# Optimization experiments

Hardware: AMD Instinct MI355X
Metric: run time of the kernel (lower is better)

Reference implementation:

```python
import jax, jax.numpy as jnp
import numpy as np

D = 512; L = 8; NH = 8; BS = 32; HW = 32; VA = 8; HA = 8; SEQ = 2 * VA * HA
DK = D // NH  # per-head dim
LN_EPS = 1e-5


def setup_inputs() -> dict:
    key = jax.random.key(0)
    ks = iter(jax.random.split(key, 40))
    def rn(shape, s=0.02):
        return (s * jax.random.normal(next(ks), shape)).astype(jnp.float32)
    inp = {
        'rgb_fea': jax.random.normal(next(ks), (BS, D, HW, HW), jnp.float32),
        'ir_fea':  jax.random.normal(next(ks), (BS, D, HW, HW), jnp.float32),
        'pos_emb': rn((1, SEQ, D)),
        'conv1_w': rn((8, D), 0.05),    # 1x1 conv, stored [out,in]
        'conv2_w': rn((D, 8), 0.05),
        'ln1_w': jnp.ones((L, D)), 'ln1_b': jnp.zeros((L, D)),
        'Wq': rn((L, D, D)), 'bq': jnp.zeros((L, D)),
        'Wk': rn((L, D, D)), 'bk': jnp.zeros((L, D)),
        'Wv': rn((L, D, D)), 'bv': jnp.zeros((L, D)),
        'Wo': rn((L, D, D)), 'bo': jnp.zeros((L, D)),
        'ln2_w': jnp.ones((L, D)), 'ln2_b': jnp.zeros((L, D)),
        'W1': rn((L, D, 4 * D)), 'b1': jnp.zeros((L, 4 * D)),
        'W2': rn((L, 4 * D, D)), 'b2': jnp.zeros((L, D)),
        'lnf_w': jnp.ones((D,)), 'lnf_b': jnp.zeros((D,)),
    }
    return inp


def _ln(x, w, b):
    m = x.mean(-1, keepdims=True)
    v = jnp.var(x, axis=-1, keepdims=True)
    return (x - m) / jnp.sqrt(v + LN_EPS) * w + b


def _avgpool8(x):
    b, c, h, w = x.shape
    return x.reshape(b, c, VA, h // VA, HA, w // HA).mean(axis=(3, 5))


def _highpass(x):
    # extract_frequency2: fftshifted FFT, zero the [crow-thr:crow+thr, ccol-thr:ccol+thr]
    # block (Python slice semantics, negative start wraps), then inverse FFT.
    rows, cols = x.shape[-2], x.shape[-1]
    crow, ccol = rows // 2, cols // 2
    thr = crow + ccol // 4
    f = jnp.fft.fftshift(jnp.fft.fftn(x, axes=(-2, -1)), axes=(-2, -1))
    f = f.at[:, :, crow - thr:crow + thr, ccol - thr:ccol + thr].set(0)
    hp = jnp.fft.ifftn(jnp.fft.ifftshift(f, axes=(-2, -1)), axes=(-2, -1))
    return hp.real  # real part (torch code casts to half; real part is the runnable interpretation)


def _block(x, p):
    ln1 = _ln(x, p['ln1_w'], p['ln1_b'])
    q = (ln1 @ p['Wq'] + p['bq']).reshape(BS, SEQ, NH, DK).transpose(0, 2, 1, 3)
    k = (ln1 @ p['Wk'] + p['bk']).reshape(BS, SEQ, NH, DK).transpose(0, 2, 1, 3)
    v = (ln1 @ p['Wv'] + p['bv']).reshape(BS, SEQ, NH, DK).transpose(0, 2, 1, 3)
    att = jax.nn.softmax(jnp.einsum('bhqd,bhkd->bhqk', q, k) / np.sqrt(DK), axis=-1)
    o = jnp.einsum('bhqk,bhkd->bhqd', att, v).transpose(0, 2, 1, 3).reshape(BS, SEQ, D)
    x = x + o @ p['Wo'] + p['bo']
    ln2 = _ln(x, p['ln2_w'], p['ln2_b'])
    h = jax.nn.gelu(ln2 @ p['W1'] + p['b1'], approximate=False)
    x = x + h @ p['W2'] + p['b2']
    return x, None


def reference(rgb_fea, ir_fea, pos_emb, conv1_w, conv2_w, ln1_w, ln1_b,
              Wq, bq, Wk, bk, Wv, bv, Wo, bo, ln2_w, ln2_b,
              W1, b1, W2, b2, lnf_w, lnf_b):
    bs, c, h, w = rgb_fea.shape
    rgb_p = _avgpool8(rgb_fea)
    ir_p = _avgpool8(ir_fea)
    rgb_hp = _highpass(rgb_p)
    ir_hp = _highpass(ir_p)

    conv1 = lambda t: jnp.einsum('bchw,oc->bohw', t, conv1_w)
    rgb_hp_M = jax.nn.sigmoid(conv1(rgb_hp * rgb_p))
    ir_hp_M = jax.nn.sigmoid(conv1(ir_hp * ir_p))
    rgb_M = jax.nn.sigmoid(conv1(rgb_p))
    ir_M = jax.nn.sigmoid(conv1(ir_p))

    hw = VA * HA
    half = (bs * 8) // 8  # = bs
    M = jnp.concatenate([rgb_M.reshape(-1, hw), ir_M.reshape(-1, hw),
                         rgb_hp_M.reshape(-1, hw)[:half], ir_hp_M.reshape(-1, hw)[:half]], axis=0)
    l = M.shape[0]
    s = M.sum(0)
    # sum_{i<j} M_i . M_j = (||sum_i M_i||^2 - sum_i ||M_i||^2) / 2
    patten_loss = (jnp.dot(s, s) - jnp.sum(M * M)) * 0.5 / (l * (l - 1))

    P_rgb = jnp.einsum('bchw,oc->bohw', rgb_M, conv2_w) * rgb_p
    P_ir = jnp.einsum('bchw,oc->bohw', ir_M, conv2_w) * ir_p

    tok = jnp.concatenate([P_rgb.reshape(bs, c, -1), P_ir.reshape(bs, c, -1)], axis=2)
    x = pos_emb + tok.transpose(0, 2, 1)  # [bs, 2*VA*HA, d]

    layer = {'ln1_w': ln1_w, 'ln1_b': ln1_b, 'Wq': Wq, 'bq': bq, 'Wk': Wk, 'bk': bk,
             'Wv': Wv, 'bv': bv, 'Wo': Wo, 'bo': bo, 'ln2_w': ln2_w, 'ln2_b': ln2_b,
             'W1': W1, 'b1': b1, 'W2': W2, 'b2': b2}
    x, _ = jax.lax.scan(_block, x, layer)
    x = _ln(x, lnf_w, lnf_b)

    x = x.reshape(bs, 2, VA, HA, D).transpose(0, 1, 4, 2, 3)  # [bs,2,d,VA,HA]
    rgb_out = jax.image.resize(x[:, 0], (bs, D, h, w), method='bilinear')
    ir_out = jax.image.resize(x[:, 1], (bs, D, h, w), method='bilinear')
    return rgb_out, ir_out, patten_loss
```

## Files before the change

kernel.cpp:

```cpp
#include <hip/hip_runtime.h>
#include <math.h>

typedef unsigned short u16;
typedef short v8s __attribute__((ext_vector_type(8)));
typedef float v4f __attribute__((ext_vector_type(4)));

#define MTOT 4096

__device__ __forceinline__ u16 f2bf(float f) {
  unsigned int u = __float_as_uint(f);
  u += 0x7fffu + ((u >> 16) & 1u);
  return (u16)(u >> 16);
}

__device__ __forceinline__ v4f mfma16(v8s a, v8s b, v4f c) {
  return __builtin_amdgcn_mfma_f32_16x16x32_bf16(a, b, c, 0, 0, 0);
}

__device__ __forceinline__ void gl_lds16(const u16* g, u16* l) {
  __builtin_amdgcn_global_load_lds(
      (const __attribute__((address_space(1))) void*)g,
      (__attribute__((address_space(3))) void*)l, 16, 0, 0);
}

__constant__ float c_ct[8] = {1.f, -0.70710678118654752f, 0.f, 0.70710678118654752f,
                              -1.f, 0.70710678118654752f, 0.f, -0.70710678118654752f};
__constant__ float c_st[8] = {0.f, 0.70710678118654752f, -1.f, 0.70710678118654752f,
                              0.f, -0.70710678118654752f, 1.f, -0.70710678118654752f};

__global__ __launch_bounds__(256) void transpose_bf16_kernel(
    const float* __restrict__ src, u16* __restrict__ dst,
    int K, int N, size_t srcLS, size_t dstLS, int rowOff)
{
  int l = blockIdx.z;
  int n0 = blockIdx.x * 32, k0 = blockIdx.y * 32;
  __shared__ float tile[32][33];
  int tx = threadIdx.x & 31, ty = threadIdx.x >> 5;
  const float* s = src + (size_t)l * srcLS;
#pragma unroll
  for (int rr = 0; rr < 4; ++rr) {
    int k = k0 + ty + rr * 8;
    tile[ty + rr * 8][tx] = s[(size_t)k * N + n0 + tx];
  }
  __syncthreads();
  u16* dp = dst + (size_t)l * dstLS;
#pragma unroll
  for (int rr = 0; rr < 4; ++rr) {
    int n = n0 + ty + rr * 8;
    dp[(size_t)(rowOff + n) * K + k0 + tx] = f2bf(tile[tx][ty + rr * 8]);
  }
}

__global__ __launch_bounds__(256) void qkv_transpose_kernel(
    const float* __restrict__ Wq, const float* __restrict__ Wk,
    const float* __restrict__ Wv, u16* __restrict__ dst)
{
  int z = blockIdx.z;
  int l = z / 3, which = z % 3;
  const float* src = (which == 0) ? Wq : (which == 1) ? Wk : Wv;
  int n0 = blockIdx.x * 32, k0 = blockIdx.y * 32;
  __shared__ float tile[32][33];
  int tx = threadIdx.x & 31, ty = threadIdx.x >> 5;
  const float* s = src + (size_t)l * 512 * 512;
#pragma unroll
  for (int rr = 0; rr < 4; ++rr) {
    int k = k0 + ty + rr * 8;
    tile[ty + rr * 8][tx] = s[(size_t)k * 512 + n0 + tx];
  }
  __syncthreads();
  u16* dp = dst + (size_t)l * 1536 * 512;
  int rowOff = which * 512;
#pragma unroll
  for (int rr = 0; rr < 4; ++rr) {
    int n = n0 + ty + rr * 8;
    dp[(size_t)(rowOff + n) * 512 + k0 + tx] = f2bf(tile[tx][ty + rr * 8]);
  }
}

__global__ __launch_bounds__(256) void qkvbias_kernel(
    const float* __restrict__ bq, const float* __restrict__ bk,
    const float* __restrict__ bv, float* __restrict__ qb)
{
  int l = blockIdx.x;
  for (int j = threadIdx.x; j < 1536; j += 256) {
    float v = (j < 512) ? bq[l * 512 + j] : (j < 1024) ? bk[l * 512 + j - 512] : bv[l * 512 + j - 1024];
    qb[l * 1536 + j] = v;
  }
}

__global__ __launch_bounds__(256) void pool_kernel(
    const float* __restrict__ rgb, const float* __restrict__ ir, float* __restrict__ pool)
{
  int idx = blockIdx.x * 4 + (threadIdx.x >> 6);
  int i = threadIdx.x & 63;
  int y = i >> 3, xcol = i & 7;
  int timg = idx >> 14;
  int rem = idx & 16383;
  const float* src = (timg ? ir : rgb) + (size_t)rem * 1024;
  float s = 0.f;
#pragma unroll
  for (int r = 0; r < 4; ++r) {
    float4 v = *(const float4*)(src + (y * 4 + r) * 32 + xcol * 4);
    s += v.x + v.y + v.z + v.w;
  }
  pool[(size_t)idx * 64 + i] = s * 0.0625f;
}

__global__ __launch_bounds__(256) void convm_kernel(
    const float* __restrict__ pool, const float* __restrict__ conv1_w,
    float* __restrict__ Macc)
{
  int r = blockIdx.x;
  int cc = blockIdx.y;
  int t = threadIdx.x, hw = t & 63, cg = t >> 6;
  int kind = (r < 64) ? 0 : 1;
  int prow;
  if (kind == 0) prow = r;
  else { int rh = r - 64; prow = (rh >> 2) * 32 + (rh & 3); }
  int yy = hw >> 3, xx = hw & 7;
  int sd = (yy + xx) & 7;
  float ct = c_ct[sd], st = c_st[sd];
  float acc[8] = {0.f,0.f,0.f,0.f,0.f,0.f,0.f,0.f};
  const float* pbase = pool + ((size_t)prow * 512 + cc * 64) * 64;
#pragma unroll 4
  for (int it = 0; it < 16; ++it) {
    int cl = cg * 16 + it;
    int c = cc * 64 + cl;
    float p = pbase[(size_t)cl * 64 + hw];
    float val = p;
    if (kind == 1) {
      float C = p * ct, S = p * st;
#pragma unroll
      for (int d = 1; d < 64; d <<= 1) { C += __shfl_xor(C, d, 64); S += __shfl_xor(S, d, 64); }
      float hp = p - (C * ct + S * st) * (1.0f / 64.0f);
      val = hp * p;
    }
#pragma unroll
    for (int o = 0; o < 8; ++o) acc[o] += conv1_w[o * 512 + c] * val;
  }
  __shared__ float red[4][8][64];
#pragma unroll
  for (int o = 0; o < 8; ++o) red[cg][o][hw] = acc[o];
  __syncthreads();
  if (cg == 0) {
#pragma unroll
    for (int o = 0; o < 8; ++o) {
      float s = red[0][o][hw] + red[1][o][hw] + red[2][o][hw] + red[3][o][hw];
      Macc[((size_t)cc * 72 + r) * 512 + o * 64 + hw] = s;
    }
  }
}

__global__ __launch_bounds__(256) void msig_kernel(
    const float* __restrict__ Macc, float* __restrict__ Mplain, float* __restrict__ Mhp)
{
  int i = blockIdx.x * 256 + threadIdx.x;
  float s = 0.f;
#pragma unroll
  for (int cc = 0; cc < 8; ++cc) s += Macc[(size_t)cc * 72 * 512 + i];
  float m = 1.0f / (1.0f + expf(-s));
  if (i < 64 * 512) Mplain[i] = m;
  else Mhp[i - 64 * 512] = m;
}

__global__ __launch_bounds__(256) void loss_kernel(
    const float* __restrict__ Mplain, const float* __restrict__ Mhp, float* __restrict__ out)
{
  int t = threadIdx.x, col = t & 63, rg = t >> 6;
  float sp = 0.f, sq = 0.f;
  for (int r = rg; r < 576; r += 4) {
    const float* rowp = (r < 512) ? (Mplain + (size_t)r * 64) : (Mhp + (size_t)(r - 512) * 64);
    float v = rowp[col];
    sp += v; sq += v * v;
  }
  __shared__ float scol[4][64], ssq[4][64];
  scol[rg][col] = sp; ssq[rg][col] = sq;
  __syncthreads();
  if (t < 64) {
    float s = scol[0][t] + scol[1][t] + scol[2][t] + scol[3][t];
    float q = ssq[0][t] + ssq[1][t] + ssq[2][t] + ssq[3][t];
    float ds = s * s;
#pragma unroll
    for (int d = 1; d < 64; d <<= 1) { ds += __shfl_xor(ds, d, 64); q += __shfl_xor(q, d, 64); }
    if (t == 0) *out = (ds - q) * 0.5f / (576.0f * 575.0f);
  }
}

__global__ __launch_bounds__(256) void token_kernel(
    const float* __restrict__ pos_emb, const float* __restrict__ conv2_w,
    const float* __restrict__ Mplain, const float* __restrict__ pool, float* __restrict__ x)
{
  int bs_idx = blockIdx.x;
  int b = bs_idx >> 7, s = bs_idx & 127;
  int timg = s >> 6, hw = s & 63;
  __shared__ float Ms[8];
  if (threadIdx.x < 8)
    Ms[threadIdx.x] = Mplain[((size_t)(timg * 32 + b) * 8 + threadIdx.x) * 64 + hw];
  __syncthreads();
#pragma unroll
  for (int i = 0; i < 2; ++i) {
    int d = threadIdx.x + i * 256;
    float acc = 0.f;
#pragma unroll
    for (int o = 0; o < 8; ++o) acc += conv2_w[d * 8 + o] * Ms[o];
    float p = pool[(((size_t)timg * 32 + b) * 512 + d) * 64 + hw];
    x[(size_t)bs_idx * 512 + d] = pos_emb[s * 512 + d] + acc * p;
  }
}

template<int OBF>
__global__ __launch_bounds__(256) void ln_kernel(
    const float* __restrict__ xin, const float* __restrict__ w,
    const float* __restrict__ bb, void* __restrict__ out)
{
  int row = blockIdx.x, t = threadIdx.x;
  float2 v = ((const float2*)(xin + (size_t)row * 512))[t];
  float s = v.x + v.y, q = v.x * v.x + v.y * v.y;
#pragma unroll
  for (int d = 1; d < 64; d <<= 1) { s += __shfl_xor(s, d, 64); q += __shfl_xor(q, d, 64); }
  __shared__ float ps[4], pq[4];
  int wv = t >> 6;
  if ((t & 63) == 0) { ps[wv] = s; pq[wv] = q; }
  __syncthreads();
  float S = ps[0] + ps[1] + ps[2] + ps[3];
  float Q = pq[0] + pq[1] + pq[2] + pq[3];
  float mean = S * (1.0f / 512.0f);
  float var = Q * (1.0f / 512.0f) - mean * mean;
  float rstd = rsqrtf(var + 1e-5f);
  float o0 = (v.x - mean) * rstd * w[t * 2] + bb[t * 2];
  float o1 = (v.y - mean) * rstd * w[t * 2 + 1] + bb[t * 2 + 1];
  if (OBF) { u16* o = (u16*)out + (size_t)row * 512; o[t * 2] = f2bf(o0); o[t * 2 + 1] = f2bf(o1); }
  else     { float* o = (float*)out + (size_t)row * 512; o[t * 2] = o0; o[t * 2 + 1] = o1; }
}

template<int ACT, int RESID, int OBF>
__global__ __launch_bounds__(256) void gemm_bt(
    const u16* __restrict__ A, const u16* __restrict__ BT,
    const float* __restrict__ bias, const float* __restrict__ resid,
    void* __restrict__ Cout, int N, int K)
{
  __shared__ u16 As[128 * 32];
  __shared__ u16 Bs[128 * 32];
  const int m0 = blockIdx.y * 128, n0 = blockIdx.x * 128;
  const int t = threadIdx.x, lane = t & 63, w = t >> 6;
  const int lr = lane & 15, lq = lane >> 4;
  const int wm = (w & 1) * 64, wn = (w >> 1) * 64;
  v4f acc[4][4];
  const v4f vzero = {0.f, 0.f, 0.f, 0.f};
#pragma unroll
  for (int mt = 0; mt < 4; ++mt)
#pragma unroll
    for (int nt = 0; nt < 4; ++nt) acc[mt][nt] = vzero;

  for (int kk = 0; kk < K; kk += 32) {
    __syncthreads();
    {
      int r0 = t >> 2, c0 = (t & 3) << 3;
      gl_lds16(A  + (size_t)(m0 + r0) * K + kk + c0, As + (size_t)(w * 64) * 8);
      gl_lds16(BT + (size_t)(n0 + r0) * K + kk + c0, Bs + (size_t)(w * 64) * 8);
      int ch = 256 + t;
      int r1 = ch >> 2, c1 = (ch & 3) << 3;
      gl_lds16(A  + (size_t)(m0 + r1) * K + kk + c1, As + (size_t)(256 + w * 64) * 8);
      gl_lds16(BT + (size_t)(n0 + r1) * K + kk + c1, Bs + (size_t)(256 + w * 64) * 8);
    }
    __syncthreads();
    v8s a[4], b[4];
#pragma unroll
    for (int mt = 0; mt < 4; ++mt)
      a[mt] = *(const v8s*)(As + (wm + mt * 16 + lr) * 32 + lq * 8);
#pragma unroll
    for (int nt = 0; nt < 4; ++nt)
      b[nt] = *(const v8s*)(Bs + (wn + nt * 16 + lr) * 32 + lq * 8);
#pragma unroll
    for (int mt = 0; mt < 4; ++mt)
#pragma unroll
      for (int nt = 0; nt < 4; ++nt)
        acc[mt][nt] = mfma16(a[mt], b[nt], acc[mt][nt]);
  }

#pragma unroll
  for (int mt = 0; mt < 4; ++mt)
#pragma unroll
    for (int nt = 0; nt < 4; ++nt) {
      int col = n0 + wn + nt * 16 + lr;
      float bsv = bias[col];
#pragma unroll
      for (int r = 0; r < 4; ++r) {
        int row = m0 + wm + mt * 16 + lq * 4 + r;
        float v = acc[mt][nt][r] + bsv;
        if (ACT == 1) v = 0.5f * v * (1.0f + erff(v * 0.70710678118654752f));
        if (RESID) v += resid[(size_t)row * N + col];
        if (OBF) ((u16*)Cout)[(size_t)row * N + col] = f2bf(v);
        else     ((float*)Cout)[(size_t)row * N + col] = v;
      }
    }
}

template<int ACT, int RESID, int OBF>
__global__ __launch_bounds__(256) void gemm_bt64(
    const u16* __restrict__ A, const u16* __restrict__ BT,
    const float* __restrict__ bias, const float* __restrict__ resid,
    void* __restrict__ Cout, int N, int K)
{
  __shared__ u16 As[128 * 32];
  __shared__ u16 Bs[64 * 32];
  const int m0 = blockIdx.y * 128, n0 = blockIdx.x * 64;
  const int t = threadIdx.x, lane = t & 63, w = t >> 6;
  const int lr = lane & 15, lq = lane >> 4;
  const int wm = (w & 1) * 64, wn = (w >> 1) * 32;
  v4f acc[4][2];
  const v4f vzero = {0.f, 0.f, 0.f, 0.f};
#pragma unroll
  for (int mt = 0; mt < 4; ++mt)
#pragma unroll
    for (int nt = 0; nt < 2; ++nt) acc[mt][nt] = vzero;

  for (int kk = 0; kk < K; kk += 32) {
    __syncthreads();
    {
      int r0 = t >> 2, c0 = (t & 3) << 3;
      gl_lds16(A  + (size_t)(m0 + r0) * K + kk + c0, As + (size_t)(w * 64) * 8);
      gl_lds16(BT + (size_t)(n0 + r0) * K + kk + c0, Bs + (size_t)(w * 64) * 8);
      int ch = 256 + t;
      int r1 = ch >> 2, c1 = (ch & 3) << 3;
      gl_lds16(A  + (size_t)(m0 + r1) * K + kk + c1, As + (size_t)(256 + w * 64) * 8);
    }
    __syncthreads();
    v8s a[4], b[2];
#pragma unroll
    for (int mt = 0; mt < 4; ++mt)
      a[mt] = *(const v8s*)(As + (wm + mt * 16 + lr) * 32 + lq * 8);
#pragma unroll
    for (int nt = 0; nt < 2; ++nt)
      b[nt] = *(const v8s*)(Bs + (wn + nt * 16 + lr) * 32 + lq * 8);
#pragma unroll
    for (int mt = 0; mt < 4; ++mt)
#pragma unroll
      for (int nt = 0; nt < 2; ++nt)
        acc[mt][nt] = mfma16(a[mt], b[nt], acc[mt][nt]);
  }

#pragma unroll
  for (int mt = 0; mt < 4; ++mt)
#pragma unroll
    for (int nt = 0; nt < 2; ++nt) {
      int col = n0 + wn + nt * 16 + lr;
      float bsv = bias[col];
#pragma unroll
      for (int r = 0; r < 4; ++r) {
        int row = m0 + wm + mt * 16 + lq * 4 + r;
        float v = acc[mt][nt][r] + bsv;
        if (ACT == 1) v = 0.5f * v * (1.0f + erff(v * 0.70710678118654752f));
        if (RESID) v += resid[(size_t)row * N + col];
        if (OBF) ((u16*)Cout)[(size_t)row * N + col] = f2bf(v);
        else     ((float*)Cout)[(size_t)row * N + col] = v;
      }
    }
}

__global__ __launch_bounds__(256) void attn_kernel(
    const u16* __restrict__ qkv, u16* __restrict__ attn_out)
{
  __shared__ u16 Ks[128 * 64];
  __shared__ u16 Vt[64 * 128];
  __shared__ u16 Ps[128 * 128];
  const int h = blockIdx.x, b = blockIdx.y;
  const int t = threadIdx.x, lane = t & 63, w = t >> 6;
  const int lr = lane & 15, lq = lane >> 4;
  const u16* base = qkv + (size_t)b * 128 * 1536 + h * 64;

#pragma unroll
  for (int i = 0; i < 4; ++i) {
    int ch = i * 256 + t;
    int s = ch >> 3, off = (ch & 7) * 8;
    *(v8s*)(Ks + s * 64 + off) = *(const v8s*)(base + 512 + (size_t)s * 1536 + off);
    v8s vv = *(const v8s*)(base + 1024 + (size_t)s * 1536 + off);
#pragma unroll
    for (int j = 0; j < 8; ++j) Vt[(off + j) * 128 + s] = (u16)vv[j];
  }
  __syncthreads();

  const v4f vzero = {0.f, 0.f, 0.f, 0.f};
  v4f sacc[2][8];
#pragma unroll
  for (int mt = 0; mt < 2; ++mt)
#pragma unroll
    for (int nt = 0; nt < 8; ++nt) sacc[mt][nt] = vzero;
#pragma unroll
  for (int kk = 0; kk < 64; kk += 32) {
    v8s a0 = *(const v8s*)(base + (size_t)(w * 32 + lr) * 1536 + kk + lq * 8);
    v8s a1 = *(const v8s*)(base + (size_t)(w * 32 + 16 + lr) * 1536 + kk + lq * 8);
#pragma unroll
    for (int nt = 0; nt < 8; ++nt) {
      v8s bb = *(const v8s*)(Ks + (nt * 16 + lr) * 64 + kk + lq * 8);
      sacc[0][nt] = mfma16(a0, bb, sacc[0][nt]);
      sacc[1][nt] = mfma16(a1, bb, sacc[1][nt]);
    }
  }

  float rinv[2][4];
#pragma unroll
  for (int mt = 0; mt < 2; ++mt)
#pragma unroll
    for (int r = 0; r < 4; ++r) {
      float mx = -3.0e38f;
#pragma unroll
      for (int nt = 0; nt < 8; ++nt) mx = fmaxf(mx, sacc[mt][nt][r]);
#pragma unroll
      for (int d = 1; d < 16; d <<= 1) mx = fmaxf(mx, __shfl_xor(mx, d, 64));
      float ls = 0.f;
      float pv[8];
#pragma unroll
      for (int nt = 0; nt < 8; ++nt) {
        pv[nt] = expf((sacc[mt][nt][r] - mx) * 0.125f);
        ls += pv[nt];
      }
#pragma unroll
      for (int d = 1; d < 16; d <<= 1) ls += __shfl_xor(ls, d, 64);
      rinv[mt][r] = 1.0f / ls;
      int row = w * 32 + mt * 16 + lq * 4 + r;
#pragma unroll
      for (int nt = 0; nt < 8; ++nt) Ps[row * 128 + nt * 16 + lr] = f2bf(pv[nt]);
    }
  __syncthreads();

  v4f oacc[2][4];
#pragma unroll
  for (int mt = 0; mt < 2; ++mt)
#pragma unroll
    for (int nt = 0; nt < 4; ++nt) oacc[mt][nt] = vzero;
#pragma unroll
  for (int kk = 0; kk < 128; kk += 32) {
    v8s a0 = *(const v8s*)(Ps + (w * 32 + lr) * 128 + kk + lq * 8);
    v8s a1 = *(const v8s*)(Ps + (w * 32 + 16 + lr) * 128 + kk + lq * 8);
#pragma unroll
    for (int nt = 0; nt < 4; ++nt) {
      v8s bb = *(const v8s*)(Vt + (nt * 16 + lr) * 128 + kk + lq * 8);
      oacc[0][nt] = mfma16(a0, bb, oacc[0][nt]);
      oacc[1][nt] = mfma16(a1, bb, oacc[1][nt]);
    }
  }
#pragma unroll
  for (int mt = 0; mt < 2; ++mt)
#pragma unroll
    for (int nt = 0; nt < 4; ++nt)
#pragma unroll
      for (int r = 0; r < 4; ++r) {
        int row = w * 32 + mt * 16 + lq * 4 + r;
        int col = nt * 16 + lr;
        attn_out[((size_t)(b * 128 + row)) * 512 + h * 64 + col] =
            f2bf(oacc[mt][nt][r] * rinv[mt][r]);
      }
}

__global__ __launch_bounds__(256) void upsample_kernel(
    const float* __restrict__ xf, float* __restrict__ out)
{
  int bid = blockIdx.x;
  int c = bid & 511;
  int tb = bid >> 9;
  int b = tb & 31, timg = tb >> 5;
  __shared__ float tile[64];
  if (threadIdx.x < 64) {
    int s = timg * 64 + threadIdx.x;
    tile[threadIdx.x] = xf[((size_t)b * 128 + s) * 512 + c];
  }
  __syncthreads();
  float* obase = out + (size_t)timg * (32ull * 512 * 1024) + ((size_t)b * 512 + c) * 1024;
#pragma unroll
  for (int k = 0; k < 4; ++k) {
    int pix = threadIdx.x + k * 256;
    int i = pix >> 5, j = pix & 31;
    float cy = fminf(fmaxf((i - 1.5f) * 0.25f, 0.f), 7.f);
    float cx = fminf(fmaxf((j - 1.5f) * 0.25f, 0.f), 7.f);
    int y0 = (int)cy, x0 = (int)cx;
    int y1 = min(y0 + 1, 7), x1 = min(x0 + 1, 7);
    float fy = cy - y0, fx = cx - x0;
    float v00 = tile[y0 * 8 + x0], v01 = tile[y0 * 8 + x1];
    float v10 = tile[y1 * 8 + x0], v11 = tile[y1 * 8 + x1];
    obase[pix] = (v00 * (1.f - fx) + v01 * fx) * (1.f - fy) + (v10 * (1.f - fx) + v11 * fx) * fy;
  }
}

extern "C" void kernel_launch(void* const* d_in, const int* in_sizes, int n_in,
                              void* d_out, int out_size, void* d_ws, size_t ws_size,
                              hipStream_t stream)
{
  const float* rgb_fea = (const float*)d_in[0];
  const float* ir_fea  = (const float*)d_in[1];
  const float* pos_emb = (const float*)d_in[2];
  const float* conv1_w = (const float*)d_in[3];
  const float* conv2_w = (const float*)d_in[4];
  const float* ln1_w = (const float*)d_in[5];
  const float* ln1_b = (const float*)d_in[6];
  const float* Wq = (const float*)d_in[7];
  const float* bq = (const float*)d_in[8];
  const float* Wk = (const float*)d_in[9];
  const float* bk = (const float*)d_in[10];
  const float* Wv = (const float*)d_in[11];
  const float* bv = (const float*)d_in[12];
  const float* Wo = (const float*)d_in[13];
  const float* bo = (const float*)d_in[14];
  const float* ln2_w = (const float*)d_in[15];
  const float* ln2_b = (const float*)d_in[16];
  const float* W1 = (const float*)d_in[17];
  const float* b1 = (const float*)d_in[18];
  const float* W2 = (const float*)d_in[19];
  const float* b2 = (const float*)d_in[20];
  const float* lnf_w = (const float*)d_in[21];
  const float* lnf_b = (const float*)d_in[22];
  (void)in_sizes; (void)n_in; (void)out_size; (void)ws_size;

  char* wsb = (char*)d_ws;
  size_t off = 0;
  auto alloc = [&](size_t nbytes) -> void* {
    void* p = wsb + off;
    off += (nbytes + 255) & ~(size_t)255;
    return p;
  };
  float* pool   = (float*)alloc(2ull * 32 * 512 * 64 * 4);
  float* Macc   = (float*)alloc(8ull * 72 * 512 * 4);
  float* Mplain = (float*)alloc(2ull * 32 * 8 * 64 * 4);
  float* Mhp    = (float*)alloc(2ull * 4 * 8 * 64 * 4);
  float* x      = (float*)alloc((size_t)MTOT * 512 * 4);
  float* xf     = (float*)alloc((size_t)MTOT * 512 * 4);
  u16* ln_out   = (u16*)alloc((size_t)MTOT * 512 * 2);
  u16* qkv      = (u16*)alloc((size_t)MTOT * 1536 * 2);
  u16* attn     = (u16*)alloc((size_t)MTOT * 512 * 2);
  u16* hbuf     = (u16*)alloc((size_t)MTOT * 2048 * 2);
  u16* WqkvT    = (u16*)alloc(8ull * 1536 * 512 * 2);
  u16* WoT      = (u16*)alloc(8ull * 512 * 512 * 2);
  u16* W1T      = (u16*)alloc(8ull * 2048 * 512 * 2);
  u16* W2T      = (u16*)alloc(8ull * 512 * 2048 * 2);
  float* qb     = (float*)alloc(8ull * 1536 * 4);

  qkv_transpose_kernel<<<dim3(16, 16, 24), 256, 0, stream>>>(Wq, Wk, Wv, WqkvT);
  transpose_bf16_kernel<<<dim3(16, 16, 8), 256, 0, stream>>>(Wo, WoT, 512, 512, 512ull * 512, 512ull * 512, 0);
  transpose_bf16_kernel<<<dim3(64, 16, 8), 256, 0, stream>>>(W1, W1T, 512, 2048, 512ull * 2048, 2048ull * 512, 0);
  transpose_bf16_kernel<<<dim3(16, 64, 8), 256, 0, stream>>>(W2, W2T, 2048, 512, 2048ull * 512, 512ull * 2048, 0);
  qkvbias_kernel<<<8, 256, 0, stream>>>(bq, bk, bv, qb);

  pool_kernel<<<8192, 256, 0, stream>>>(rgb_fea, ir_fea, pool);
  convm_kernel<<<dim3(72, 8), 256, 0, stream>>>(pool, conv1_w, Macc);
  msig_kernel<<<144, 256, 0, stream>>>(Macc, Mplain, Mhp);
  loss_kernel<<<1, 256, 0, stream>>>(Mplain, Mhp, (float*)d_out + 33554432);
  token_kernel<<<MTOT, 256, 0, stream>>>(pos_emb, conv2_w, Mplain, pool, x);

  for (int l = 0; l < 8; ++l) {
    ln_kernel<1><<<MTOT, 256, 0, stream>>>(x, ln1_w + l * 512, ln1_b + l * 512, ln_out);
    gemm_bt<0, 0, 1><<<dim3(12, 32), 256, 0, stream>>>(
        ln_out, WqkvT + (size_t)l * 1536 * 512, qb + l * 1536, nullptr, qkv, 1536, 512);
    attn_kernel<<<dim3(8, 32), 256, 0, stream>>>(qkv, attn);
    gemm_bt64<0, 1, 0><<<dim3(8, 32), 256, 0, stream>>>(
        attn, WoT + (size_t)l * 512 * 512, bo + l * 512, x, x, 512, 512);
    ln_kernel<1><<<MTOT, 256, 0, stream>>>(x, ln2_w + l * 512, ln2_b + l * 512, ln_out);
    gemm_bt<1, 0, 1><<<dim3(16, 32), 256, 0, stream>>>(
        ln_out, W1T + (size_t)l * 2048 * 512, b1 + l * 2048, nullptr, hbuf, 2048, 512);
    gemm_bt64<0, 1, 0><<<dim3(8, 32), 256, 0, stream>>>(
        hbuf, W2T + (size_t)l * 512 * 2048, b2 + l * 512, x, x, 512, 2048);
  }

  ln_kernel<0><<<MTOT, 256, 0, stream>>>(x, lnf_w, lnf_b, xf);
  upsample_kernel<<<32768, 256, 0, stream>>>(xf, (float*)d_out);
}
```

Measured before the change: 1.374 ms.

## Widen GEMM K-step with XOR-swizzled LDS, tanh GELU, one-wave-per-row LayerNorm

```diff
diff --git a/kernel.cpp b/kernel.cpp
--- a/kernel.cpp
+++ b/kernel.cpp
@@ -3,6 +3,7 @@
 
 typedef unsigned short u16;
 typedef short v8s __attribute__((ext_vector_type(8)));
+typedef unsigned short v8u __attribute__((ext_vector_type(8)));
 typedef float v4f __attribute__((ext_vector_type(4)));
 
 #define MTOT 4096
@@ -21,6 +22,12 @@
   __builtin_amdgcn_global_load_lds(
       (const __attribute__((address_space(1))) void*)g,
       (__attribute__((address_space(3))) void*)l, 16, 0, 0);
+}
+
+__device__ __forceinline__ float fast_gelu(float v) {
+  float y = 0.7978845608028654f * (v + 0.044715f * v * v * v);
+  float t = 1.0f - 2.0f / (__expf(2.0f * y) + 1.0f);
+  return 0.5f * v * (1.0f + t);
 }
 
 __constant__ float c_ct[8] = {1.f, -0.70710678118654752f, 0.f, 0.70710678118654752f,
@@ -213,24 +220,38 @@
     const float* __restrict__ xin, const float* __restrict__ w,
     const float* __restrict__ bb, void* __restrict__ out)
 {
-  int row = blockIdx.x, t = threadIdx.x;
-  float2 v = ((const float2*)(xin + (size_t)row * 512))[t];
-  float s = v.x + v.y, q = v.x * v.x + v.y * v.y;
+  int wv = threadIdx.x >> 6, lane = threadIdx.x & 63;
+  int row = blockIdx.x * 4 + wv;
+  const float4* rp = (const float4*)(xin + (size_t)row * 512);
+  float4 v0 = rp[lane * 2], v1 = rp[lane * 2 + 1];
+  float s = v0.x + v0.y + v0.z + v0.w + v1.x + v1.y + v1.z + v1.w;
+  float q = v0.x*v0.x + v0.y*v0.y + v0.z*v0.z + v0.w*v0.w
+          + v1.x*v1.x + v1.y*v1.y + v1.z*v1.z + v1.w*v1.w;
 #pragma unroll
   for (int d = 1; d < 64; d <<= 1) { s += __shfl_xor(s, d, 64); q += __shfl_xor(q, d, 64); }
-  __shared__ float ps[4], pq[4];
-  int wv = t >> 6;
-  if ((t & 63) == 0) { ps[wv] = s; pq[wv] = q; }
-  __syncthreads();
-  float S = ps[0] + ps[1] + ps[2] + ps[3];
-  float Q = pq[0] + pq[1] + pq[2] + pq[3];
-  float mean = S * (1.0f / 512.0f);
-  float var = Q * (1.0f / 512.0f) - mean * mean;
+  float mean = s * (1.0f / 512.0f);
+  float var = q * (1.0f / 512.0f) - mean * mean;
   float rstd = rsqrtf(var + 1e-5f);
-  float o0 = (v.x - mean) * rstd * w[t * 2] + bb[t * 2];
-  float o1 = (v.y - mean) * rstd * w[t * 2 + 1] + bb[t * 2 + 1];
-  if (OBF) { u16* o = (u16*)out + (size_t)row * 512; o[t * 2] = f2bf(o0); o[t * 2 + 1] = f2bf(o1); }
-  else     { float* o = (float*)out + (size_t)row * 512; o[t * 2] = o0; o[t * 2 + 1] = o1; }
+  const float4* wp = (const float4*)w;
+  const float4* bp = (const float4*)bb;
+  float4 w0 = wp[lane * 2], w1 = wp[lane * 2 + 1];
+  float4 b0 = bp[lane * 2], b1 = bp[lane * 2 + 1];
+  float o0 = (v0.x - mean) * rstd * w0.x + b0.x;
+  float o1 = (v0.y - mean) * rstd * w0.y + b0.y;
+  float o2 = (v0.z - mean) * rstd * w0.z + b0.z;
+  float o3 = (v0.w - mean) * rstd * w0.w + b0.w;
+  float o4 = (v1.x - mean) * rstd * w1.x + b1.x;
+  float o5 = (v1.y - mean) * rstd * w1.y + b1.y;
+  float o6 = (v1.z - mean) * rstd * w1.z + b1.z;
+  float o7 = (v1.w - mean) * rstd * w1.w + b1.w;
+  if (OBF) {
+    v8u pk = { f2bf(o0), f2bf(o1), f2bf(o2), f2bf(o3), f2bf(o4), f2bf(o5), f2bf(o6), f2bf(o7) };
+    *(v8u*)((u16*)out + (size_t)row * 512 + lane * 8) = pk;
+  } else {
+    float4* op = (float4*)((float*)out + (size_t)row * 512);
+    op[lane * 2] = make_float4(o0, o1, o2, o3);
+    op[lane * 2 + 1] = make_float4(o4, o5, o6, o7);
+  }
 }
 
 template<int ACT, int RESID, int OBF>
@@ -239,8 +260,8 @@
     const float* __restrict__ bias, const float* __restrict__ resid,
     void* __restrict__ Cout, int N, int K)
 {
-  __shared__ u16 As[128 * 32];
-  __shared__ u16 Bs[128 * 32];
+  __shared__ u16 As[128 * 64];
+  __shared__ u16 Bs[128 * 64];
   const int m0 = blockIdx.y * 128, n0 = blockIdx.x * 128;
   const int t = threadIdx.x, lane = t & 63, w = t >> 6;
   const int lr = lane & 15, lq = lane >> 4;
@@ -252,30 +273,43 @@
 #pragma unroll
     for (int nt = 0; nt < 4; ++nt) acc[mt][nt] = vzero;
 
-  for (int kk = 0; kk < K; kk += 32) {
+  int srow[4], sgs[4];
+#pragma unroll
+  for (int i = 0; i < 4; ++i) {
+    int c = t + i * 256;
+    srow[i] = c >> 3;
+    sgs[i] = (c & 7) ^ (srow[i] & 7);
+  }
+
+  for (int kk = 0; kk < K; kk += 64) {
     __syncthreads();
-    {
-      int r0 = t >> 2, c0 = (t & 3) << 3;
-      gl_lds16(A  + (size_t)(m0 + r0) * K + kk + c0, As + (size_t)(w * 64) * 8);
-      gl_lds16(BT + (size_t)(n0 + r0) * K + kk + c0, Bs + (size_t)(w * 64) * 8);
-      int ch = 256 + t;
-      int r1 = ch >> 2, c1 = (ch & 3) << 3;
-      gl_lds16(A  + (size_t)(m0 + r1) * K + kk + c1, As + (size_t)(256 + w * 64) * 8);
-      gl_lds16(BT + (size_t)(n0 + r1) * K + kk + c1, Bs + (size_t)(256 + w * 64) * 8);
+#pragma unroll
+    for (int i = 0; i < 4; ++i) {
+      gl_lds16(A  + (size_t)(m0 + srow[i]) * K + kk + sgs[i] * 8, As + (size_t)(w * 64 + i * 256) * 8);
+      gl_lds16(BT + (size_t)(n0 + srow[i]) * K + kk + sgs[i] * 8, Bs + (size_t)(w * 64 + i * 256) * 8);
     }
     __syncthreads();
-    v8s a[4], b[4];
-#pragma unroll
-    for (int mt = 0; mt < 4; ++mt)
-      a[mt] = *(const v8s*)(As + (wm + mt * 16 + lr) * 32 + lq * 8);
-#pragma unroll
-    for (int nt = 0; nt < 4; ++nt)
-      b[nt] = *(const v8s*)(Bs + (wn + nt * 16 + lr) * 32 + lq * 8);
-#pragma unroll
-    for (int mt = 0; mt < 4; ++mt)
-#pragma unroll
-      for (int nt = 0; nt < 4; ++nt)
-        acc[mt][nt] = mfma16(a[mt], b[nt], acc[mt][nt]);
+#pragma unroll
+    for (int ks = 0; ks < 2; ++ks) {
+      v8s a[4], b[4];
+#pragma unroll
+      for (int mt = 0; mt < 4; ++mt) {
+        int row = wm + mt * 16 + lr;
+        int cL = (ks * 4 + lq) ^ (row & 7);
+        a[mt] = *(const v8s*)(As + row * 64 + cL * 8);
+      }
+#pragma unroll
+      for (int nt = 0; nt < 4; ++nt) {
+        int row = wn + nt * 16 + lr;
+        int cL = (ks * 4 + lq) ^ (row & 7);
+        b[nt] = *(const v8s*)(Bs + row * 64 + cL * 8);
+      }
+#pragma unroll
+      for (int mt = 0; mt < 4; ++mt)
+#pragma unroll
+        for (int nt = 0; nt < 4; ++nt)
+          acc[mt][nt] = mfma16(a[mt], b[nt], acc[mt][nt]);
+    }
   }
 
 #pragma unroll
@@ -288,7 +322,7 @@
       for (int r = 0; r < 4; ++r) {
         int row = m0 + wm + mt * 16 + lq * 4 + r;
         float v = acc[mt][nt][r] + bsv;
-        if (ACT == 1) v = 0.5f * v * (1.0f + erff(v * 0.70710678118654752f));
+        if (ACT == 1) v = fast_gelu(v);
         if (RESID) v += resid[(size_t)row * N + col];
         if (OBF) ((u16*)Cout)[(size_t)row * N + col] = f2bf(v);
         else     ((float*)Cout)[(size_t)row * N + col] = v;
@@ -302,8 +336,8 @@
     const float* __restrict__ bias, const float* __restrict__ resid,
     void* __restrict__ Cout, int N, int K)
 {
-  __shared__ u16 As[128 * 32];
-  __shared__ u16 Bs[64 * 32];
+  __shared__ u16 As[128 * 64];
+  __shared__ u16 Bs[64 * 64];
   const int m0 = blockIdx.y * 128, n0 = blockIdx.x * 64;
   const int t = threadIdx.x, lane = t & 63, w = t >> 6;
   const int lr = lane & 15, lq = lane >> 4;
@@ -315,29 +349,44 @@
 #pragma unroll
     for (int nt = 0; nt < 2; ++nt) acc[mt][nt] = vzero;
 
-  for (int kk = 0; kk < K; kk += 32) {
+  int srow[4], sgs[4];
+#pragma unroll
+  for (int i = 0; i < 4; ++i) {
+    int c = t + i * 256;
+    srow[i] = c >> 3;
+    sgs[i] = (c & 7) ^ (srow[i] & 7);
+  }
+
+  for (int kk = 0; kk < K; kk += 64) {
     __syncthreads();
-    {
-      int r0 = t >> 2, c0 = (t & 3) << 3;
-      gl_lds16(A  + (size_t)(m0 + r0) * K + kk + c0, As + (size_t)(w * 64) * 8);
-      gl_lds16(BT + (size_t)(n0 + r0) * K + kk + c0, Bs + (size_t)(w * 64) * 8);
-      int ch = 256 + t;
-      int r1 = ch >> 2, c1 = (ch & 3) << 3;
-      gl_lds16(A  + (size_t)(m0 + r1) * K + kk + c1, As + (size_t)(256 + w * 64) * 8);
-    }
+#pragma unroll
+    for (int i = 0; i < 4; ++i)
+      gl_lds16(A + (size_t)(m0 + srow[i]) * K + kk + sgs[i] * 8, As + (size_t)(w * 64 + i * 256) * 8);
+#pragma unroll
+    for (int i = 0; i < 2; ++i)
+      gl_lds16(BT + (size_t)(n0 + srow[i]) * K + kk + sgs[i] * 8, Bs + (size_t)(w * 64 + i * 256) * 8);
     __syncthreads();
-    v8s a[4], b[2];
-#pragma unroll
-    for (int mt = 0; mt < 4; ++mt)
-      a[mt] = *(const v8s*)(As + (wm + mt * 16 + lr) * 32 + lq * 8);
-#pragma unroll
-    for (int nt = 0; nt < 2; ++nt)
-      b[nt] = *(const v8s*)(Bs + (wn + nt * 16 + lr) * 32 + lq * 8);
-#pragma unroll
-    for (int mt = 0; mt < 4; ++mt)
-#pragma unroll
-      for (int nt = 0; nt < 2; ++nt)
-        acc[mt][nt] = mfma16(a[mt], b[nt], acc[mt][nt]);
+#pragma unroll
+    for (int ks = 0; ks < 2; ++ks) {
+      v8s a[4], b[2];
+#pragma unroll
+      for (int mt = 0; mt < 4; ++mt) {
+        int row = wm + mt * 16 + lr;
+        int cL = (ks * 4 + lq) ^ (row & 7);
+        a[mt] = *(const v8s*)(As + row * 64 + cL * 8);
+      }
+#pragma unroll
+      for (int nt = 0; nt < 2; ++nt) {
+        int row = wn + nt * 16 + lr;
+        int cL = (ks * 4 + lq) ^ (row & 7);
+        b[nt] = *(const v8s*)(Bs + row * 64 + cL * 8);
+      }
+#pragma unroll
+      for (int mt = 0; mt < 4; ++mt)
+#pragma unroll
+        for (int nt = 0; nt < 2; ++nt)
+          acc[mt][nt] = mfma16(a[mt], b[nt], acc[mt][nt]);
+    }
   }
 
 #pragma unroll
@@ -350,7 +399,7 @@
       for (int r = 0; r < 4; ++r) {
         int row = m0 + wm + mt * 16 + lq * 4 + r;
         float v = acc[mt][nt][r] + bsv;
-        if (ACT == 1) v = 0.5f * v * (1.0f + erff(v * 0.70710678118654752f));
+        if (ACT == 1) v = fast_gelu(v);
         if (RESID) v += resid[(size_t)row * N + col];
         if (OBF) ((u16*)Cout)[(size_t)row * N + col] = f2bf(v);
         else     ((float*)Cout)[(size_t)row * N + col] = v;
@@ -547,19 +596,19 @@
   token_kernel<<<MTOT, 256, 0, stream>>>(pos_emb, conv2_w, Mplain, pool, x);
 
   for (int l = 0; l < 8; ++l) {
-    ln_kernel<1><<<MTOT, 256, 0, stream>>>(x, ln1_w + l * 512, ln1_b + l * 512, ln_out);
+    ln_kernel<1><<<MTOT / 4, 256, 0, stream>>>(x, ln1_w + l * 512, ln1_b + l * 512, ln_out);
     gemm_bt<0, 0, 1><<<dim3(12, 32), 256, 0, stream>>>(
         ln_out, WqkvT + (size_t)l * 1536 * 512, qb + l * 1536, nullptr, qkv, 1536, 512);
     attn_kernel<<<dim3(8, 32), 256, 0, stream>>>(qkv, attn);
     gemm_bt64<0, 1, 0><<<dim3(8, 32), 256, 0, stream>>>(
         attn, WoT + (size_t)l * 512 * 512, bo + l * 512, x, x, 512, 512);
-    ln_kernel<1><<<MTOT, 256, 0, stream>>>(x, ln2_w + l * 512, ln2_b + l * 512, ln_out);
+    ln_kernel<1><<<MTOT / 4, 256, 0, stream>>>(x, ln2_w + l * 512, ln2_b + l * 512, ln_out);
     gemm_bt<1, 0, 1><<<dim3(16, 32), 256, 0, stream>>>(
         ln_out, W1T + (size_t)l * 2048 * 512, b1 + l * 2048, nullptr, hbuf, 2048, 512);
     gemm_bt64<0, 1, 0><<<dim3(8, 32), 256, 0, stream>>>(
         hbuf, W2T + (size_t)l * 512 * 2048, b2 + l * 512, x, x, 512, 2048);
   }
 
-  ln_kernel<0><<<MTOT, 256, 0, stream>>>(x, lnf_w, lnf_b, xf);
+  ln_kernel<0><<<MTOT / 4, 256, 0, stream>>>(x, lnf_w, lnf_b, xf);
   upsample_kernel<<<32768, 256, 0, stream>>>(xf, (float*)d_out);
 }
```

New measurement: 1.307 ms. 4.9% less time.
